# Optimization experiments

Measured on AMD Instinct MI355X. Metric: run time of the kernel, lower is better.

The kernel has to match this reference:

```python
import jax, jax.numpy as jnp
import numpy as np

LAYER_SHAPES = [(256, 64, 56, 56), (256, 128, 28, 28), (256, 256, 14, 14), (256, 512, 7, 7)]
NUM_REF = 2000


def _lid_layer(ref, q, k):
    """MLE LID estimate (Ma et al.) per query row.
    ref: [R, C] reference activations; q: [B, C] pooled query activations.
    """
    # Euclidean cdist via the expansion ||q||^2 - 2 q.ref^T + ||ref||^2
    d2 = (jnp.sum(q * q, axis=1, keepdims=True)
          - 2.0 * (q @ ref.T)
          + jnp.sum(ref * ref, axis=1)[None, :])            # [B, R]
    d = jnp.sqrt(jnp.maximum(d2, 0.0))
    # smallest k+1 distances, drop the nearest (mirrors sorted[:,1:k+1])
    neg_topk = jax.lax.top_k(-d, k + 1)[0]                   # descending in -d => ascending d
    dk = -neg_topk[:, 1:k + 1]                               # [B, k], ascending
    # LID = -k / sum_i log(d_i / d_k)
    return -k / jnp.sum(jnp.log(dk / dk[:, -1:]), axis=1)    # [B]


def setup_inputs() -> dict:
    key = jax.random.key(0)
    ks = jax.random.split(key, 12)
    inp = {}
    for i, shp in enumerate(LAYER_SHAPES):
        inp[f"feat{i}"] = jax.random.normal(ks[i], shp, dtype=jnp.float32)
        inp[f"ref{i}"] = jax.random.normal(ks[4 + i], (NUM_REF, shp[1]), dtype=jnp.float32)
    inp["reg_w"] = jax.random.normal(ks[8], (1, 4), dtype=jnp.float32)
    inp["reg_b"] = jax.random.normal(ks[9], (1,), dtype=jnp.float32)
    inp["k"] = 20
    return inp


def reference(feat0, feat1, feat2, feat3, ref0, ref1, ref2, ref3, reg_w, reg_b, k):
    feats = [feat0, feat1, feat2, feat3]
    refs = [ref0, ref1, ref2, ref3]
    lid_scores = []
    for f, r in zip(feats, refs):
        fq = jnp.mean(f.reshape(f.shape[0], f.shape[1], -1), axis=2)  # [B, C]
        lid_scores.append(_lid_layer(r, fq, k))
    lid_feat = jnp.stack(lid_scores, axis=1)                 # [B, num_layers]
    logit = lid_feat @ reg_w.T + reg_b                        # [B, 1]
    return jax.nn.sigmoid(logit)[:, 0]
```

## Files before the change

kernel.cpp:

```cpp
#include <hip/hip_runtime.h>
#include <cmath>

#define WS_FQ_OFF      0u
#define WS_R2_OFF      245760u
#define WS_LID_OFF     253760u
#define WS_G_OFF       262144u
#define G_LAYER_STRIDE 512000u
#define NREF           2000

__global__ __launch_bounds__(256) void pool_kernel(const float* __restrict__ feat,
                                                   float* __restrict__ fq,
                                                   int HW, float invHW) {
    int w = threadIdx.x >> 6, lane = threadIdx.x & 63;
    size_t row = (size_t)blockIdx.x * 4 + w;
    const float* p = feat + row * (size_t)HW;
    float s = 0.f;
    if ((HW & 3) == 0) {
        const float4* p4 = (const float4*)p;
        int n4 = HW >> 2;
        for (int i = lane; i < n4; i += 64) {
            float4 v = p4[i];
            s += (v.x + v.y) + (v.z + v.w);
        }
    } else {
        for (int i = lane; i < HW; i += 64) s += p[i];
    }
    #pragma unroll
    for (int off = 32; off; off >>= 1) s += __shfl_down(s, off, 64);
    if (lane == 0) fq[row] = s * invHW;
}

__global__ __launch_bounds__(256) void r2_kernel(const float* __restrict__ ref0,
                                                 const float* __restrict__ ref1,
                                                 const float* __restrict__ ref2,
                                                 const float* __restrict__ ref3,
                                                 float* __restrict__ r2_all) {
    int layer = blockIdx.y;
    int w = threadIdx.x >> 6, lane = threadIdx.x & 63;
    int r = blockIdx.x * 4 + w;
    if (r >= NREF) return;
    const float* rp; int C;
    switch (layer) {
        case 0:  rp = ref0; C = 64;  break;
        case 1:  rp = ref1; C = 128; break;
        case 2:  rp = ref2; C = 256; break;
        default: rp = ref3; C = 512; break;
    }
    const float4* row = (const float4*)(rp + (size_t)r * C);
    int n4 = C >> 2;
    float s = 0.f;
    for (int i = lane; i < n4; i += 64) {
        float4 v = row[i];
        s += v.x*v.x + v.y*v.y + v.z*v.z + v.w*v.w;
    }
    #pragma unroll
    for (int off = 32; off; off >>= 1) s += __shfl_down(s, off, 64);
    if (lane == 0) r2_all[layer * NREF + r] = s;
}

#define BM 64
#define BN 64
#define BK 32
#define LDT 68
__global__ __launch_bounds__(256) void gemm_qr(const float* __restrict__ A,
                                               const float* __restrict__ B,
                                               float* __restrict__ G,
                                               int K, int N) {
    __shared__ __align__(16) float As[BK * LDT];
    __shared__ __align__(16) float Bs[BK * LDT];
    int t = threadIdx.x;
    int tq = t & 15, tr = t >> 4;
    int m0 = blockIdx.x * BM;
    int n0 = blockIdx.y * BN;
    int row0 = t >> 3;
    int kc4  = t & 7;
    float acc[4][4] = {};

    for (int k0 = 0; k0 < K; k0 += BK) {
        #pragma unroll
        for (int half = 0; half < 2; ++half) {
            int row = row0 + half * 32;
            float4 av = *(const float4*)(A + (size_t)(m0 + row) * K + k0 + kc4 * 4);
            int brow = n0 + row;
            float4 bv = make_float4(0.f, 0.f, 0.f, 0.f);
            if (brow < N) bv = *(const float4*)(B + (size_t)brow * K + k0 + kc4 * 4);
            As[(kc4*4 + 0) * LDT + row] = av.x;
            As[(kc4*4 + 1) * LDT + row] = av.y;
            As[(kc4*4 + 2) * LDT + row] = av.z;
            As[(kc4*4 + 3) * LDT + row] = av.w;
            Bs[(kc4*4 + 0) * LDT + row] = bv.x;
            Bs[(kc4*4 + 1) * LDT + row] = bv.y;
            Bs[(kc4*4 + 2) * LDT + row] = bv.z;
            Bs[(kc4*4 + 3) * LDT + row] = bv.w;
        }
        __syncthreads();
        #pragma unroll
        for (int kk = 0; kk < BK; ++kk) {
            float4 a = *(const float4*)&As[kk * LDT + tq * 4];
            float4 b = *(const float4*)&Bs[kk * LDT + tr * 4];
            acc[0][0] += a.x*b.x; acc[0][1] += a.x*b.y; acc[0][2] += a.x*b.z; acc[0][3] += a.x*b.w;
            acc[1][0] += a.y*b.x; acc[1][1] += a.y*b.y; acc[1][2] += a.y*b.z; acc[1][3] += a.y*b.w;
            acc[2][0] += a.z*b.x; acc[2][1] += a.z*b.y; acc[2][2] += a.z*b.z; acc[2][3] += a.z*b.w;
            acc[3][0] += a.w*b.x; acc[3][1] += a.w*b.y; acc[3][2] += a.w*b.z; acc[3][3] += a.w*b.w;
        }
        __syncthreads();
    }

    int rbase = n0 + tr * 4;
    if (rbase < N) {
        #pragma unroll
        for (int i = 0; i < 4; ++i) {
            float4 o = make_float4(acc[i][0], acc[i][1], acc[i][2], acc[i][3]);
            *(float4*)(G + (size_t)(m0 + tq*4 + i) * N + rbase) = o;
        }
    }
}

__global__ __launch_bounds__(256) void topk_lid_kernel(const float* __restrict__ fq_all,
                                                       const float* __restrict__ G_all,
                                                       const float* __restrict__ r2_all,
                                                       float* __restrict__ lid,
                                                       const int* __restrict__ kptr) {
    __shared__ float d2s[NREF];
    __shared__ float wsum[4];
    __shared__ unsigned long long redmin[4];
    __shared__ float sel[64];

    const int Cs[4]  = {64, 128, 256, 512};
    const int fqo[4] = {0, 16384, 49152, 114688};

    int b = blockIdx.x, layer = blockIdx.y;
    int t = threadIdx.x;
    int k = kptr[0];
    if (k > 63) k = 63;
    int C = Cs[layer];
    const float* fq = fq_all + fqo[layer] + (size_t)b * C;
    const float* G  = G_all + (size_t)layer * G_LAYER_STRIDE + (size_t)b * NREF;
    const float* r2 = r2_all + layer * NREF;

    float s = 0.f;
    for (int c = t; c < C; c += 256) { float v = fq[c]; s += v * v; }
    #pragma unroll
    for (int off = 32; off; off >>= 1) s += __shfl_down(s, off, 64);
    if ((t & 63) == 0) wsum[t >> 6] = s;
    __syncthreads();
    float q2 = wsum[0] + wsum[1] + wsum[2] + wsum[3];

    for (int r = t; r < NREF; r += 256) {
        float v = q2 - 2.f * G[r] + r2[r];
        d2s[r] = v > 0.f ? v : 0.f;
    }
    __syncthreads();

    int nsel = k + 1;
    for (int it = 0; it < nsel; ++it) {
        unsigned long long best = ~0ull;
        for (int r = t; r < NREF; r += 256) {
            unsigned long long key = ((unsigned long long)__float_as_uint(d2s[r]) << 32)
                                     | (unsigned)r;
            if (key < best) best = key;
        }
        #pragma unroll
        for (int off = 32; off; off >>= 1) {
            unsigned long long o = __shfl_down(best, off, 64);
            if (o < best) best = o;
        }
        if ((t & 63) == 0) redmin[t >> 6] = best;
        __syncthreads();
        if (t == 0) {
            unsigned long long m = redmin[0];
            #pragma unroll
            for (int w = 1; w < 4; ++w) if (redmin[w] < m) m = redmin[w];
            int idx = (int)(m & 0xffffffffu);
            sel[it] = __uint_as_float((unsigned)(m >> 32));
            d2s[idx] = __uint_as_float(0x7f800000u);
        }
        __syncthreads();
    }

    if (t == 0) {
        float lk = logf(sel[k]);
        float ssum = 0.f;
        for (int i = 1; i <= k; ++i) ssum += (logf(sel[i]) - lk);
        lid[b * 4 + layer] = -(float)k / (0.5f * ssum);
    }
}

__global__ __launch_bounds__(256) void head_kernel(const float* __restrict__ lid,
                                                   const float* __restrict__ w,
                                                   const float* __restrict__ bias,
                                                   float* __restrict__ out) {
    int b = threadIdx.x;
    float acc = bias[0];
    #pragma unroll
    for (int l = 0; l < 4; ++l) acc += lid[b * 4 + l] * w[l];
    out[b] = 1.f / (1.f + expf(-acc));
}

extern "C" void kernel_launch(void* const* d_in, const int* in_sizes, int n_in,
                              void* d_out, int out_size, void* d_ws, size_t ws_size,
                              hipStream_t stream) {
    const float* feat[4] = {(const float*)d_in[0], (const float*)d_in[2],
                            (const float*)d_in[4], (const float*)d_in[6]};
    const float* ref[4]  = {(const float*)d_in[1], (const float*)d_in[3],
                            (const float*)d_in[5], (const float*)d_in[7]};
    const float* reg_w = (const float*)d_in[8];
    const float* reg_b = (const float*)d_in[9];
    const int*   kptr  = (const int*)d_in[10];

    float* ws     = (float*)d_ws;
    float* fq_all = ws + WS_FQ_OFF;
    float* r2_all = ws + WS_R2_OFF;
    float* lid    = ws + WS_LID_OFF;
    float* G_all  = ws + WS_G_OFF;

    const int Cs[4]  = {64, 128, 256, 512};
    const int HWs[4] = {3136, 784, 196, 49};
    const int fqo[4] = {0, 16384, 49152, 114688};

    for (int l = 0; l < 4; ++l) {
        int rows = 256 * Cs[l];
        pool_kernel<<<rows / 4, 256, 0, stream>>>(feat[l], fq_all + fqo[l],
                                                  HWs[l], 1.0f / (float)HWs[l]);
    }
    r2_kernel<<<dim3(NREF / 4, 4), 256, 0, stream>>>(ref[0], ref[1], ref[2], ref[3], r2_all);
    for (int l = 0; l < 4; ++l) {
        gemm_qr<<<dim3(256 / BM, (NREF + BN - 1) / BN), 256, 0, stream>>>(
            fq_all + fqo[l], ref[l], G_all + (size_t)l * G_LAYER_STRIDE, Cs[l], NREF);
    }
    topk_lid_kernel<<<dim3(256, 4), 256, 0, stream>>>(fq_all, G_all, r2_all, lid, kptr);
    head_kernel<<<1, 256, 0, stream>>>(lid, reg_w, reg_b, (float*)d_out);
}
```

Baseline: 521.3 us.

## Replace iterative top-k with radix histogram select and split-K GEMM partials

The top-k stage no longer runs k+1 block-wide argmin passes with two barriers each. It builds a 2048-bin histogram of distance bit patterns, finds the bin holding the (k+1)-th smallest value, sums logs of everything below it directly, and resolves only the candidates in that bin with a warp-level selection. The nearest distance is subtracted via a tracked minimum. Separately, the GEMM is split along K into 64-wide chunks written as partial sums and reduced in the top-k kernel, which raises GEMM parallelism at the cost of extra workspace traffic.

```diff
diff --git a/kernel.cpp b/kernel.cpp
--- a/kernel.cpp
+++ b/kernel.cpp
@@ -5,8 +5,9 @@
 #define WS_R2_OFF      245760u
 #define WS_LID_OFF     253760u
 #define WS_G_OFF       262144u
-#define G_LAYER_STRIDE 512000u
+#define G_CHUNK_STRIDE 512000u
 #define NREF           2000
+#define KC             64
 
 __global__ __launch_bounds__(256) void pool_kernel(const float* __restrict__ feat,
                                                    float* __restrict__ fq,
@@ -64,7 +65,7 @@
 #define LDT 68
 __global__ __launch_bounds__(256) void gemm_qr(const float* __restrict__ A,
                                                const float* __restrict__ B,
-                                               float* __restrict__ G,
+                                               float* __restrict__ Gp,
                                                int K, int N) {
     __shared__ __align__(16) float As[BK * LDT];
     __shared__ __align__(16) float Bs[BK * LDT];
@@ -72,11 +73,12 @@
     int tq = t & 15, tr = t >> 4;
     int m0 = blockIdx.x * BM;
     int n0 = blockIdx.y * BN;
+    int kb = blockIdx.z * KC;
     int row0 = t >> 3;
     int kc4  = t & 7;
     float acc[4][4] = {};
 
-    for (int k0 = 0; k0 < K; k0 += BK) {
+    for (int k0 = kb; k0 < kb + KC; k0 += BK) {
         #pragma unroll
         for (int half = 0; half < 2; ++half) {
             int row = row0 + half * 32;
@@ -106,12 +108,13 @@
         __syncthreads();
     }
 
+    float* Gout = Gp + (size_t)blockIdx.z * G_CHUNK_STRIDE;
     int rbase = n0 + tr * 4;
     if (rbase < N) {
         #pragma unroll
         for (int i = 0; i < 4; ++i) {
             float4 o = make_float4(acc[i][0], acc[i][1], acc[i][2], acc[i][3]);
-            *(float4*)(G + (size_t)(m0 + tq*4 + i) * N + rbase) = o;
+            *(float4*)(Gout + (size_t)(m0 + tq*4 + i) * N + rbase) = o;
         }
     }
 }
@@ -121,68 +124,164 @@
                                                        const float* __restrict__ r2_all,
                                                        float* __restrict__ lid,
                                                        const int* __restrict__ kptr) {
-    __shared__ float d2s[NREF];
-    __shared__ float wsum[4];
-    __shared__ unsigned long long redmin[4];
-    __shared__ float sel[64];
-
-    const int Cs[4]  = {64, 128, 256, 512};
-    const int fqo[4] = {0, 16384, 49152, 114688};
+    __shared__ __align__(16) float d2s[NREF];
+    __shared__ unsigned hist[2048];
+    __shared__ float redq[4], redm[4], redl[4];
+    __shared__ unsigned long long red8[4];
+    __shared__ int sh_B, sh_cbelow, sh_cnt;
+    __shared__ float sh_dmin;
+
+    const int Cs[4]   = {64, 128, 256, 512};
+    const int fqo[4]  = {0, 16384, 49152, 114688};
+    const int nchs[4] = {1, 2, 4, 8};
+    const int coff[4] = {0, 1, 3, 7};
 
     int b = blockIdx.x, layer = blockIdx.y;
     int t = threadIdx.x;
+    int lane = t & 63, w = t >> 6;
     int k = kptr[0];
-    if (k > 63) k = 63;
+    if (k + 1 > NREF) k = NREF - 1;
+    unsigned K1 = (unsigned)(k + 1);
     int C = Cs[layer];
+    int nch = nchs[layer];
     const float* fq = fq_all + fqo[layer] + (size_t)b * C;
-    const float* G  = G_all + (size_t)layer * G_LAYER_STRIDE + (size_t)b * NREF;
+    const float* Gb = G_all + (size_t)coff[layer] * G_CHUNK_STRIDE + (size_t)b * NREF;
     const float* r2 = r2_all + layer * NREF;
-
+    const float INF = __uint_as_float(0x7f800000u);
+
+    for (int i = t; i < 2048; i += 256) hist[i] = 0u;
+    if (t == 0) sh_cnt = 0;
     float s = 0.f;
     for (int c = t; c < C; c += 256) { float v = fq[c]; s += v * v; }
     #pragma unroll
     for (int off = 32; off; off >>= 1) s += __shfl_down(s, off, 64);
-    if ((t & 63) == 0) wsum[t >> 6] = s;
+    if (lane == 0) redq[w] = s;
     __syncthreads();
-    float q2 = wsum[0] + wsum[1] + wsum[2] + wsum[3];
-
-    for (int r = t; r < NREF; r += 256) {
-        float v = q2 - 2.f * G[r] + r2[r];
-        d2s[r] = v > 0.f ? v : 0.f;
-    }
+    float q2 = redq[0] + redq[1] + redq[2] + redq[3];
+
+    float minv = INF;
+    for (int i = t; i < NREF / 4; i += 256) {
+        float4 g = make_float4(0.f, 0.f, 0.f, 0.f);
+        for (int c = 0; c < nch; ++c) {
+            float4 v = *(const float4*)(Gb + (size_t)c * G_CHUNK_STRIDE + i * 4);
+            g.x += v.x; g.y += v.y; g.z += v.z; g.w += v.w;
+        }
+        float4 rr = *(const float4*)(r2 + i * 4);
+        float d0 = q2 - 2.f * g.x + rr.x; d0 = d0 > 0.f ? d0 : 0.f;
+        float d1 = q2 - 2.f * g.y + rr.y; d1 = d1 > 0.f ? d1 : 0.f;
+        float d2_ = q2 - 2.f * g.z + rr.z; d2_ = d2_ > 0.f ? d2_ : 0.f;
+        float d3 = q2 - 2.f * g.w + rr.w; d3 = d3 > 0.f ? d3 : 0.f;
+        *(float4*)(d2s + i * 4) = make_float4(d0, d1, d2_, d3);
+        atomicAdd(&hist[__float_as_uint(d0) >> 20], 1u);
+        atomicAdd(&hist[__float_as_uint(d1) >> 20], 1u);
+        atomicAdd(&hist[__float_as_uint(d2_) >> 20], 1u);
+        atomicAdd(&hist[__float_as_uint(d3) >> 20], 1u);
+        minv = fminf(minv, fminf(fminf(d0, d1), fminf(d2_, d3)));
+    }
+    #pragma unroll
+    for (int off = 32; off; off >>= 1) minv = fminf(minv, __shfl_down(minv, off, 64));
+    if (lane == 0) redm[w] = minv;
     __syncthreads();
 
-    int nsel = k + 1;
-    for (int it = 0; it < nsel; ++it) {
-        unsigned long long best = ~0ull;
-        for (int r = t; r < NREF; r += 256) {
-            unsigned long long key = ((unsigned long long)__float_as_uint(d2s[r]) << 32)
-                                     | (unsigned)r;
-            if (key < best) best = key;
-        }
+    if (t < 64) {
+        unsigned p = 0;
+        int base = t * 32;
+        #pragma unroll 4
+        for (int i = 0; i < 32; ++i) p += hist[base + i];
+        unsigned cum = p;
         #pragma unroll
-        for (int off = 32; off; off >>= 1) {
-            unsigned long long o = __shfl_down(best, off, 64);
-            if (o < best) best = o;
-        }
-        if ((t & 63) == 0) redmin[t >> 6] = best;
-        __syncthreads();
+        for (int off = 1; off < 64; off <<= 1) {
+            unsigned o = __shfl_up(cum, off, 64);
+            if (t >= off) cum += o;
+        }
+        unsigned excl = cum - p;
+        if (excl < K1 && K1 <= cum) {
+            unsigned run = excl;
+            int binB = base;
+            for (int i = 0; i < 32; ++i) {
+                unsigned c = hist[base + i];
+                if (run + c >= K1) { binB = base + i; break; }
+                run += c;
+            }
+            sh_B = binB;
+            sh_cbelow = (int)run;
+        }
+        if (t == 0) sh_dmin = fminf(fminf(redm[0], redm[1]), fminf(redm[2], redm[3]));
+    }
+    __syncthreads();
+
+    int B = sh_B;
+    float* cand = (float*)hist;
+    float lsum = 0.f;
+    for (int i = t; i < NREF; i += 256) {
+        float v = d2s[i];
+        int bin = (int)(__float_as_uint(v) >> 20);
+        if (bin < B) {
+            lsum += logf(v);
+        } else if (bin == B) {
+            int pos = atomicAdd(&sh_cnt, 1);
+            cand[pos] = v;
+        }
+    }
+    #pragma unroll
+    for (int off = 32; off; off >>= 1) lsum += __shfl_down(lsum, off, 64);
+    if (lane == 0) redl[w] = lsum;
+    __syncthreads();
+
+    int cnt = sh_cnt;
+    int m = (int)K1 - sh_cbelow;
+    if (cnt <= 64) {
+        if (t < 64) {
+            float mv = (t < cnt) ? cand[t] : INF;
+            float csum = 0.f, dk = 0.f;
+            for (int it = 0; it < m; ++it) {
+                float x = mv;
+                #pragma unroll
+                for (int off = 32; off; off >>= 1) x = fminf(x, __shfl_xor(x, off, 64));
+                csum += logf(x);
+                dk = x;
+                unsigned long long ball = __ballot(mv == x);
+                int src = __ffsll(ball) - 1;
+                if (t == src) mv = INF;
+            }
+            if (t == 0) {
+                float lsum_tot = redl[0] + redl[1] + redl[2] + redl[3];
+                float denom = 0.5f * (lsum_tot + csum - logf(sh_dmin) - (float)k * logf(dk));
+                lid[b * 4 + layer] = -(float)k / denom;
+            }
+        }
+    } else {
+        float csum = 0.f, dk = 0.f;
+        for (int it = 0; it < m; ++it) {
+            unsigned long long best = ~0ull;
+            for (int i = t; i < cnt; i += 256) {
+                unsigned long long key =
+                    ((unsigned long long)__float_as_uint(cand[i]) << 32) | (unsigned)i;
+                if (key < best) best = key;
+            }
+            #pragma unroll
+            for (int off = 32; off; off >>= 1) {
+                unsigned long long o = __shfl_down(best, off, 64);
+                if (o < best) best = o;
+            }
+            if (lane == 0) red8[w] = best;
+            __syncthreads();
+            unsigned long long mm = red8[0];
+            #pragma unroll
+            for (int ww = 1; ww < 4; ++ww) if (red8[ww] < mm) mm = red8[ww];
+            float v = __uint_as_float((unsigned)(mm >> 32));
+            if (t == 0) {
+                csum += logf(v);
+                dk = v;
+                cand[(int)(mm & 0xffffffffu)] = INF;
+            }
+            __syncthreads();
+        }
         if (t == 0) {
-            unsigned long long m = redmin[0];
-            #pragma unroll
-            for (int w = 1; w < 4; ++w) if (redmin[w] < m) m = redmin[w];
-            int idx = (int)(m & 0xffffffffu);
-            sel[it] = __uint_as_float((unsigned)(m >> 32));
-            d2s[idx] = __uint_as_float(0x7f800000u);
-        }
-        __syncthreads();
-    }
-
-    if (t == 0) {
-        float lk = logf(sel[k]);
-        float ssum = 0.f;
-        for (int i = 1; i <= k; ++i) ssum += (logf(sel[i]) - lk);
-        lid[b * 4 + layer] = -(float)k / (0.5f * ssum);
+            float lsum_tot = redl[0] + redl[1] + redl[2] + redl[3];
+            float denom = 0.5f * (lsum_tot + csum - logf(sh_dmin) - (float)k * logf(dk));
+            lid[b * 4 + layer] = -(float)k / denom;
+        }
     }
 }
 
@@ -212,11 +311,12 @@
     float* fq_all = ws + WS_FQ_OFF;
     float* r2_all = ws + WS_R2_OFF;
     float* lid    = ws + WS_LID_OFF;
-    float* G_all  = ws + WS_G_OFF;
-
-    const int Cs[4]  = {64, 128, 256, 512};
-    const int HWs[4] = {3136, 784, 196, 49};
-    const int fqo[4] = {0, 16384, 49152, 114688};
+    float* G_part = ws + WS_G_OFF;
+
+    const int Cs[4]   = {64, 128, 256, 512};
+    const int HWs[4]  = {3136, 784, 196, 49};
+    const int fqo[4]  = {0, 16384, 49152, 114688};
+    const int coff[4] = {0, 1, 3, 7};
 
     for (int l = 0; l < 4; ++l) {
         int rows = 256 * Cs[l];
@@ -225,9 +325,10 @@
     }
     r2_kernel<<<dim3(NREF / 4, 4), 256, 0, stream>>>(ref[0], ref[1], ref[2], ref[3], r2_all);
     for (int l = 0; l < 4; ++l) {
-        gemm_qr<<<dim3(256 / BM, (NREF + BN - 1) / BN), 256, 0, stream>>>(
-            fq_all + fqo[l], ref[l], G_all + (size_t)l * G_LAYER_STRIDE, Cs[l], NREF);
-    }
-    topk_lid_kernel<<<dim3(256, 4), 256, 0, stream>>>(fq_all, G_all, r2_all, lid, kptr);
+        int chunks = Cs[l] / KC;
+        gemm_qr<<<dim3(256 / BM, (NREF + BN - 1) / BN, chunks), 256, 0, stream>>>(
+            fq_all + fqo[l], ref[l], G_part + (size_t)coff[l] * G_CHUNK_STRIDE, Cs[l], NREF);
+    }
+    topk_lid_kernel<<<dim3(256, 4), 256, 0, stream>>>(fq_all, G_part, r2_all, lid, kptr);
     head_kernel<<<1, 256, 0, stream>>>(lid, reg_w, reg_b, (float*)d_out);
 }
```

Result: faster. 481.5 us (-7.6%).
